# Performance work log

Measured on AMD Instinct MI355X. Metric: run time of the kernel, lower is better.

Reference implementation:

```python
import jax, jax.numpy as jnp
import numpy as np
from jax import lax

B, T, D, H = 128, 129, 128, 64  # batch, window, input_size (num driving series), hidden_size
Tm1 = T - 1


def setup_inputs() -> dict:
    key = jax.random.key(0)
    ks = jax.random.split(key, 11)
    s = 0.05
    return {
        "input_data": jax.random.normal(ks[0], (B, Tm1, D), jnp.float32),
        "W_ehs_w": jax.random.normal(ks[1], (Tm1, 2 * H), jnp.float32) * s,
        "W_ehs_b": jax.random.normal(ks[2], (Tm1,), jnp.float32) * s,
        "U_e_w": jax.random.normal(ks[3], (Tm1, Tm1), jnp.float32) * s,
        "U_e_b": jax.random.normal(ks[4], (Tm1,), jnp.float32) * s,
        "v_e_w": jax.random.normal(ks[5], (1, Tm1), jnp.float32) * s,
        "v_e_b": jax.random.normal(ks[6], (1,), jnp.float32) * s,
        "W_ih": jax.random.normal(ks[7], (4 * H, D), jnp.float32) * s,
        "W_hh": jax.random.normal(ks[8], (4 * H, H), jnp.float32) * s,
        "b_ih": jax.random.normal(ks[9], (4 * H,), jnp.float32) * s,
        "b_hh": jax.random.normal(ks[10], (4 * H,), jnp.float32) * s,
    }


def reference(input_data, W_ehs_w, W_ehs_b, U_e_w, U_e_b, v_e_w, v_e_b, W_ih, W_hh, b_ih, b_hh):
    # input_data: [B, T-1, D]
    dt = input_data.dtype
    # U_e applied to each driving series' full history; constant across t.
    # x_k = input.permute(0,2,1) -> [B, D, T-1]; Linear: x @ W.T + b
    x_perm = jnp.transpose(input_data, (0, 2, 1))            # [B, D, T-1]
    Ue_x = jnp.einsum("bdt,st->bds", x_perm, U_e_w) + U_e_b  # [B, D, T-1]

    def step(carry, x_t):
        h, c = carry                                          # each [B, H]
        # In the torch code (h,c) are broadcast identically over the D axis,
        # so compute W_ehs once per batch row and broadcast.
        hc = jnp.concatenate([h, c], axis=-1)                 # [B, 2H]
        we = hc @ W_ehs_w.T + W_ehs_b                         # [B, T-1]
        z = jnp.tanh(we[:, None, :] + Ue_x)                   # [B, D, T-1]
        v = z @ v_e_w[0] + v_e_b[0]                           # [B, D]
        a = jax.nn.softmax(v, axis=1)                         # softmax over drivers
        x_hat = a * x_t                                       # [B, D]
        # single LSTM step (torch gate order: i, f, g, o)
        gates = x_hat @ W_ih.T + b_ih + h @ W_hh.T + b_hh     # [B, 4H]
        i, f, g, o = jnp.split(gates, 4, axis=1)
        c_new = jax.nn.sigmoid(f) * c + jax.nn.sigmoid(i) * jnp.tanh(g)
        h_new = jax.nn.sigmoid(o) * jnp.tanh(c_new)
        return (h_new, c_new), (x_hat, h_new)

    h0 = jnp.zeros((input_data.shape[0], H), dt)
    c0 = jnp.zeros((input_data.shape[0], H), dt)
    xs = jnp.transpose(input_data, (1, 0, 2))                 # time-major [T-1, B, D]
    _, (xw, he) = lax.scan(step, (h0, c0), xs)
    input_weighted = jnp.transpose(xw, (1, 0, 2))             # [B, T-1, D]
    input_encoded = jnp.transpose(he, (1, 0, 2))              # [B, T-1, H]
    return input_weighted, input_encoded
```

## Files before the change

kernel.cpp:

```cpp
#include <hip/hip_runtime.h>
#include <hip/hip_bf16.h>
#include <hip/hip_fp16.h>

#define NB 128
#define NT 128
#define ND 128
#define NH 64
#define NTH 1024
#define ESTR 144

typedef float f32x2 __attribute__((ext_vector_type(2)));
typedef _Float16 f16x2 __attribute__((ext_vector_type(2)));

__device__ __forceinline__ float fexp2(float x) { return __builtin_amdgcn_exp2f(x); }
__device__ __forceinline__ float frcp (float x) { return __builtin_amdgcn_rcpf(x); }

template<int CTRL>
__device__ __forceinline__ float dppadd(float v) {
  return v + __int_as_float(__builtin_amdgcn_update_dpp(
      0, __float_as_int(v), CTRL, 0xF, 0xF, true));
}
__device__ __forceinline__ float sum16(float v) {
  v = dppadd<0xB1>(v);
  v = dppadd<0x4E>(v);
  v = dppadd<0x141>(v);
  v = dppadd<0x140>(v);
  return v;
}

__device__ __forceinline__ unsigned short f2bf(float f) {
  unsigned u = __float_as_uint(f);
  u += 0x7fffu + ((u >> 16) & 1u);
  return (unsigned short)(u >> 16);
}
__device__ __forceinline__ float blo(unsigned u) { return __uint_as_float(u << 16); }
__device__ __forceinline__ float bhi(unsigned u) { return __uint_as_float(u & 0xffff0000u); }

__device__ __forceinline__ __half2 uh(unsigned u) {
  union { unsigned u; __half2 h; } x; x.u = u; return x.h;
}
__device__ __forceinline__ unsigned hu(__half2 h) {
  union { unsigned u; __half2 h; } x; x.h = h; return x.u;
}
__device__ __forceinline__ f16x2 uh2(unsigned u) {
  union { unsigned u; f16x2 h; } x; x.u = u; return x.h;
}
__device__ __forceinline__ unsigned pkf16(float lo, float hi) {
  return hu(__halves2half2(__float2half_rn(lo), __float2half_rn(hi)));
}

__device__ __forceinline__ float dot2(unsigned a, unsigned b, float c) {
#if __has_builtin(__builtin_amdgcn_fdot2)
  return __builtin_amdgcn_fdot2(uh2(a), uh2(b), c, false);
#else
  const __half2 p = __hmul2(uh(a), uh(b));
  return c + __low2float(p) + __high2float(p);
#endif
}

#define PIN(v) asm volatile("" : "+v"(v))

__global__ __launch_bounds__(NTH)
__attribute__((amdgpu_waves_per_eu(4, 4)))
void darnn_enc(
    const float* __restrict__ x,
    const float* __restrict__ Wehs,
    const float* __restrict__ behs,
    const float* __restrict__ Ue,
    const float* __restrict__ Ueb,
    const float* __restrict__ vew,
    const float* __restrict__ Wih,
    const float* __restrict__ Whh,
    const float* __restrict__ bih,
    const float* __restrict__ bhh,
    float* __restrict__ out)
{
  constexpr float C2  = 2.88539008177792681f;
  constexpr float L2E = 1.44269504088896340f;

  __shared__ __align__(16) float          xh[NT][ND];
  __shared__ __align__(16) unsigned short Ebt[ND][ESTR];
  __shared__ __align__(16) float          hbuf[NT][NH];
  __shared__ __align__(16) unsigned       hcpk[2][8][12];
  __shared__ __align__(16) float          cq[2][16][6];
  __shared__ __align__(16) float          wvm[16][12];
  __shared__ __align__(16) unsigned       xpk[16][12];
  __shared__ __align__(16) float          part64[64];
  __shared__ __align__(16) float          rsb[NT];

  const int b    = blockIdx.x;
  const int tid  = threadIdx.x;
  const int lane = tid & 63;
  const int wid  = tid >> 6;
  const float* xb = x + b * (NT * ND);

#pragma unroll
  for (int i = 0; i < 4; ++i) {
    const int f = i * 1024 + tid;
    const int t = f >> 5, c = (f & 31) << 2;
    *reinterpret_cast<float4*>(&xh[t][c]) =
        *reinterpret_cast<const float4*>(xb + t * ND + c);
  }
  float (*UeTc)[33] = reinterpret_cast<float(*)[33]>(&hbuf[0][0]);
  __syncthreads();

  {
    const int SQ = tid & 31;
    const int DQ = tid >> 5;
    float acc[16];
#pragma unroll
    for (int i = 0; i < 16; ++i) acc[i] = 0.f;
    for (int c = 0; c < 4; ++c) {
      {
        const int ss = 32 * c + DQ;
        const int t4 = 4 * SQ;
        const float4 u4 = *reinterpret_cast<const float4*>(Ue + ss * NT + t4);
        UeTc[t4 + 0][DQ] = u4.x;
        UeTc[t4 + 1][DQ] = u4.y;
        UeTc[t4 + 2][DQ] = u4.z;
        UeTc[t4 + 3][DQ] = u4.w;
      }
      __syncthreads();
#pragma unroll 4
      for (int t = 0; t < NT; ++t) {
        const float4 xv = *reinterpret_cast<const float4*>(&xh[t][4 * DQ]);
        const float u = UeTc[t][SQ];
        acc[4*c+0] = fmaf(xv.x, u, acc[4*c+0]);
        acc[4*c+1] = fmaf(xv.y, u, acc[4*c+1]);
        acc[4*c+2] = fmaf(xv.z, u, acc[4*c+2]);
        acc[4*c+3] = fmaf(xv.w, u, acc[4*c+3]);
      }
      __syncthreads();
    }
#pragma unroll
    for (int c = 0; c < 4; ++c) {
      const int ss = SQ + 32 * c;
      const float ub = Ueb[ss];
#pragma unroll
      for (int di = 0; di < 4; ++di) {
        const float e = fexp2(C2 * (acc[4*c+di] + ub));
        Ebt[4*DQ + di][ss] = f2bf(e);
      }
    }
  }
  __syncthreads();

  if (tid < 192) (&hcpk[0][0][0])[tid] = 0u;
  if (tid < 192) (&cq[0][0][0])[tid] = 0.f;

  const int s_a = tid >> 3, r_a = tid & 7;
  unsigned wehs_p[8];
#pragma unroll
  for (int i = 0; i < 4; ++i) {
    const float4 v4 = *reinterpret_cast<const float4*>(Wehs + s_a * 128 + r_a * 16 + 4 * i);
    wehs_p[2*i]   = pkf16(C2 * v4.x, C2 * v4.y);
    wehs_p[2*i+1] = pkf16(C2 * v4.z, C2 * v4.w);
  }
  float behs_r = C2 * behs[s_a];

  const int s_l = lane & 15;
  const int dp  = lane >> 4;
  const int d0  = 8 * wid + 2 * dp;
  f32x2 mv[4];
  {
    const float4 va = *reinterpret_cast<const float4*>(vew + 8 * s_l);
    const float4 vb = *reinterpret_cast<const float4*>(vew + 8 * s_l + 4);
    const float k = -2.f * L2E;
    mv[0] = (f32x2){k * va.x, k * va.y};
    mv[1] = (f32x2){k * va.z, k * va.w};
    mv[2] = (f32x2){k * vb.x, k * vb.y};
    mv[3] = (f32x2){k * vb.z, k * vb.w};
  }
  f32x2 er2[8];
  {
    const int4 ea = *reinterpret_cast<const int4*>(&Ebt[d0][8 * s_l]);
    const int4 eb = *reinterpret_cast<const int4*>(&Ebt[d0 + 1][8 * s_l]);
    er2[0] = (f32x2){blo((unsigned)ea.x), bhi((unsigned)ea.x)};
    er2[1] = (f32x2){blo((unsigned)ea.y), bhi((unsigned)ea.y)};
    er2[2] = (f32x2){blo((unsigned)ea.z), bhi((unsigned)ea.z)};
    er2[3] = (f32x2){blo((unsigned)ea.w), bhi((unsigned)ea.w)};
    er2[4] = (f32x2){blo((unsigned)eb.x), bhi((unsigned)eb.x)};
    er2[5] = (f32x2){blo((unsigned)eb.y), bhi((unsigned)eb.y)};
    er2[6] = (f32x2){blo((unsigned)eb.z), bhi((unsigned)eb.z)};
    er2[7] = (f32x2){blo((unsigned)eb.w), bhi((unsigned)eb.w)};
  }

  const int kk = lane >> 4, cD = lane & 15;
  const int kD = 4 * wid + kk;
  unsigned wx2[16], wh2[8];
  float b4[4];
#pragma unroll
  for (int g = 0; g < 4; ++g) {
    const int j = 64 * g + kD;
    const float4 u0 = *reinterpret_cast<const float4*>(Wih + j * 128 + 8 * cD);
    const float4 u1 = *reinterpret_cast<const float4*>(Wih + j * 128 + 8 * cD + 4);
    wx2[4*g]   = pkf16(u0.x, u0.y);
    wx2[4*g+1] = pkf16(u0.z, u0.w);
    wx2[4*g+2] = pkf16(u1.x, u1.y);
    wx2[4*g+3] = pkf16(u1.z, u1.w);
    const float4 u2 = *reinterpret_cast<const float4*>(Whh + j * 64 + 4 * cD);
    wh2[2*g]   = pkf16(u2.x, u2.y);
    wh2[2*g+1] = pkf16(u2.z, u2.w);
    b4[g] = bih[j] + bhh[j];
  }

#pragma unroll
  for (int i = 0; i < 8; ++i) PIN(wehs_p[i]);
#pragma unroll
  for (int i = 0; i < 8; ++i) PIN(er2[i]);
#pragma unroll
  for (int i = 0; i < 4; ++i) PIN(mv[i]);
#pragma unroll
  for (int i = 0; i < 16; ++i) PIN(wx2[i]);
#pragma unroll
  for (int i = 0; i < 8; ++i) PIN(wh2[i]);
#pragma unroll
  for (int g = 0; g < 4; ++g) PIN(b4[g]);
  PIN(behs_r);

  __syncthreads();

#define STEP(T, P) do {                                                        \
    const float2 xv = *reinterpret_cast<const float2*>(&xh[(T)][d0]);          \
    float c_old;                                                               \
     {                          \
      const int4 q0 = *reinterpret_cast<const int4*>(&hcpk[(P)][r_a][0]);      \
      const int4 q1 = *reinterpret_cast<const int4*>(&hcpk[(P)][r_a][4]);      \
      c_old = cq[(P)][wid][kk];    \
      float a0 = 0.f, a1 = 0.f;                                                \
      a0 = dot2((unsigned)q0.x, wehs_p[0], a0);                                \
      a1 = dot2((unsigned)q0.y, wehs_p[1], a1);                                \
      a0 = dot2((unsigned)q0.z, wehs_p[2], a0);                                \
      a1 = dot2((unsigned)q0.w, wehs_p[3], a1);                                \
      a0 = dot2((unsigned)q1.x, wehs_p[4], a0);                                \
      a1 = dot2((unsigned)q1.y, wehs_p[5], a1);                                \
      a0 = dot2((unsigned)q1.z, wehs_p[6], a0);                                \
      a1 = dot2((unsigned)q1.w, wehs_p[7], a1);                                \
      float a = a0 + a1;                                                       \
      a = dppadd<0xB1>(a);                                                     \
      a = dppadd<0x4E>(a);                                                     \
      a = dppadd<0x141>(a);                                                    \
      if (r_a == 0) wvm[s_a >> 3][s_a & 7] = fexp2(a + behs_r);                \
    }                                                                          \
    __syncthreads();                                                           \
    int2 hh;                                                                   \
     {                      \
      const float4 wa = *reinterpret_cast<const float4*>(&wvm[s_l][0]);        \
      const float4 wb = *reinterpret_cast<const float4*>(&wvm[s_l][4]);        \
      hh = *reinterpret_cast<const int2*>(&hcpk[(P)][cD >> 2][2 * (cD & 3)]);  \
      const f32x2 one2 = {1.f, 1.f};                                           \
      const f32x2 w01 = {wa.x, wa.y}, w23 = {wa.z, wa.w};                      \
      const f32x2 w45 = {wb.x, wb.y}, w67 = {wb.z, wb.w};                      \
      f32x2 ac0 = {0.f, 0.f}, ac0b = {0.f, 0.f};                               \
      f32x2 ac1 = {0.f, 0.f}, ac1b = {0.f, 0.f};                               \
      BSTEP(w01, er2[0], mv[0], ac0);                                          \
      BSTEP(w23, er2[1], mv[1], ac0b);                                         \
      BSTEP(w45, er2[2], mv[2], ac0);                                          \
      BSTEP(w67, er2[3], mv[3], ac0b);                                         \
      BSTEP(w01, er2[4], mv[0], ac1);                                          \
      BSTEP(w23, er2[5], mv[1], ac1b);                                         \
      BSTEP(w45, er2[6], mv[2], ac1);                                          \
      BSTEP(w67, er2[7], mv[3], ac1b);                                         \
      const f32x2 sv0 = ac0 + ac0b;                                            \
      const f32x2 sv1 = ac1 + ac1b;                                            \
      float s0 = sum16(sv0.x + sv0.y);                                         \
      float s1 = sum16(sv1.x + sv1.y);                                         \
      const float e0 = fexp2(s0);                                              \
      const float e1 = fexp2(s1);                                              \
      if (s_l == 0) {                                                          \
        part64[4 * wid + dp] = e0 + e1;                                        \
        xpk[wid][dp] = pkf16(e0 * xv.x, e1 * xv.y);                            \
        *reinterpret_cast<float2*>(&xh[(T)][d0]) =                             \
            make_float2(e0 * xv.x, e1 * xv.y);                                 \
      }                                                                        \
    }                                                                          \
    __syncthreads();                                                           \
     {     \
      const int4 xq = *reinterpret_cast<const int4*>(&xpk[cD][0]);             \
      float sx[4], sh[4];                                                      \
      _Pragma("unroll")                                                        \
      for (int g = 0; g < 4; ++g) {                                            \
        float s = 0.f;                                                         \
        s = dot2((unsigned)xq.x, wx2[4*g],   s);                               \
        s = dot2((unsigned)xq.y, wx2[4*g+1], s);                               \
        s = dot2((unsigned)xq.z, wx2[4*g+2], s);                               \
        s = dot2((unsigned)xq.w, wx2[4*g+3], s);                               \
        sx[g] = s;                                                             \
        float h = 0.f;                                                         \
        h = dot2((unsigned)hh.x, wh2[2*g],   h);                               \
        h = dot2((unsigned)hh.y, wh2[2*g+1], h);                               \
        sh[g] = h;                                                             \
      }                                                                        \
      float tot = part64[lane];                                                \
      tot = sum16(tot);                                                        \
      tot += __int_as_float(__builtin_amdgcn_ds_swizzle(__float_as_int(tot), 0x401F)); \
      tot += __shfl_xor(tot, 32);                                              \
      const float rs = frcp(tot);                                              \
      float ac[4];                                                             \
      _Pragma("unroll")                                                        \
      for (int g = 0; g < 4; ++g) ac[g] = sum16(fmaf(sx[g], rs, sh[g]));       \
      const float gi = ac[0] + b4[0];                                          \
      const float gf = ac[1] + b4[1];                                          \
      const float gG = ac[2] + b4[2];                                          \
      const float go = ac[3] + b4[3];                                          \
      const float si = frcp(1.f + fexp2(-L2E * gi));                           \
      const float sf = frcp(1.f + fexp2(-L2E * gf));                           \
      const float tg = 1.f - 2.f * frcp(1.f + fexp2(C2 * gG));                 \
      const float cn = fmaf(sf, c_old, si * tg);                               \
      const float so = frcp(1.f + fexp2(-L2E * go));                           \
      const float tc = 1.f - 2.f * frcp(1.f + fexp2(C2 * cn));                 \
      const float hn = so * tc;                                                \
      if (cD == 0) {                                                           \
        __half* Hb = reinterpret_cast<__half*>(&hcpk[(P) ^ 1][0][0]);          \
        Hb[(kD >> 4) * 24 + (kD & 15)]       = __float2half_rn(hn);            \
        Hb[(4 + (kD >> 4)) * 24 + (kD & 15)] = __float2half_rn(cn);            \
        cq[(P) ^ 1][wid][kk] = cn;                                             \
        hbuf[(T)][kD] = hn;                                                    \
      }                                                                        \
      if (tid == 0) rsb[(T)] = rs;                                             \
    }                                                                          \
    __syncthreads();                                                           \
  } while (0)

#define BSTEP(W, E, M, ACC) do {                                   \
    f32x2 q_ = __builtin_elementwise_fma(W, E, one2);              \
    f32x2 r_; r_.x = frcp(q_.x); r_.y = frcp(q_.y);                \
    ACC = __builtin_elementwise_fma(M, r_, ACC);                   \
  } while (0)

  for (int t = 0; t < NT; t += 2) {
    STEP(t, 0);
    STEP(t + 1, 1);
  }
#undef BSTEP
#undef STEP

#pragma unroll
  for (int i = 0; i < 4; ++i) {
    const int f = i * 1024 + tid;
    const int t = f >> 5, c = (f & 31) << 2;
    float4 v = *reinterpret_cast<const float4*>(&xh[t][c]);
    const float rs = rsb[t];
    v.x *= rs; v.y *= rs; v.z *= rs; v.w *= rs;
    *reinterpret_cast<float4*>(out + b * (NT * ND) + t * ND + c) = v;
  }
  float* out2 = out + NB * (NT * ND) + b * (NT * NH);
#pragma unroll
  for (int i = 0; i < 2; ++i) {
    const int f = i * 1024 + tid;
    const int t = f >> 4, c = (f & 15) << 2;
    *reinterpret_cast<float4*>(out2 + t * NH + c) =
        *reinterpret_cast<const float4*>(&hbuf[t][c]);
  }
}

extern "C" void kernel_launch(void* const* d_in, const int* in_sizes, int n_in,
                              void* d_out, int out_size, void* d_ws, size_t ws_size,
                              hipStream_t stream) {
  const float* x    = (const float*)d_in[0];
  const float* Wehs = (const float*)d_in[1];
  const float* behs = (const float*)d_in[2];
  const float* Ue   = (const float*)d_in[3];
  const float* Ueb  = (const float*)d_in[4];
  const float* vew  = (const float*)d_in[5];
  const float* Wih  = (const float*)d_in[7];
  const float* Whh  = (const float*)d_in[8];
  const float* bih  = (const float*)d_in[9];
  const float* bhh  = (const float*)d_in[10];
  float* out = (float*)d_out;

  darnn_enc<<<NB, NTH, 0, stream>>>(x, Wehs, behs, Ue, Ueb, vew, Wih, Whh, bih, bhh, out);
}
```

Baseline: 258.7 us.

## Compute Ue·x directly into per-thread registers, dropping the bf16 LDS staging buffer

The precomputation of exp(2·(U_e x + b)) is restructured. Each thread now computes exactly the (d, s) elements it later needs, using packed f32x2 FMAs. U_e is transposed once into the xh LDS region with a permuted column layout, and x is read straight from global memory. This removes the Ebt bf16 buffer, the bf16 round-trip, and the four chunked passes with their extra barriers. It also keeps the exponentials in full fp32 rather than bf16. The cost is that every thread re-reads x from global/L2 (2 floats per t) and performs redundant work across the lanes that share d.

Result: faster. 250.5 us (-3.2%).

```diff
diff --git a/kernel.cpp b/kernel.cpp
--- a/kernel.cpp
+++ b/kernel.cpp
@@ -7,7 +7,6 @@
 #define ND 128
 #define NH 64
 #define NTH 1024
-#define ESTR 144
 
 typedef float f32x2 __attribute__((ext_vector_type(2)));
 typedef _Float16 f16x2 __attribute__((ext_vector_type(2)));
@@ -27,14 +26,6 @@
   v = dppadd<0x140>(v);
   return v;
 }
-
-__device__ __forceinline__ unsigned short f2bf(float f) {
-  unsigned u = __float_as_uint(f);
-  u += 0x7fffu + ((u >> 16) & 1u);
-  return (unsigned short)(u >> 16);
-}
-__device__ __forceinline__ float blo(unsigned u) { return __uint_as_float(u << 16); }
-__device__ __forceinline__ float bhi(unsigned u) { return __uint_as_float(u & 0xffff0000u); }
 
 __device__ __forceinline__ __half2 uh(unsigned u) {
   union { unsigned u; __half2 h; } x; x.u = u; return x.h;
@@ -79,7 +70,6 @@
   constexpr float L2E = 1.44269504088896340f;
 
   __shared__ __align__(16) float          xh[NT][ND];
-  __shared__ __align__(16) unsigned short Ebt[ND][ESTR];
   __shared__ __align__(16) float          hbuf[NT][NH];
   __shared__ __align__(16) unsigned       hcpk[2][8][12];
   __shared__ __align__(16) float          cq[2][16][6];
@@ -94,6 +84,62 @@
   const int wid  = tid >> 6;
   const float* xb = x + b * (NT * ND);
 
+  const int s_l = lane & 15;
+  const int dp  = lane >> 4;
+  const int d0  = 8 * wid + 2 * dp;
+
+  float (*UeT)[ND] = reinterpret_cast<float(*)[ND]>(&xh[0][0]);
+  {
+    const int s_r = tid & 127;
+    const int t_q = tid >> 7;
+    const int col = 64 * ((s_r >> 2) & 1) + 4 * (s_r >> 3) + (s_r & 3);
+#pragma unroll
+    for (int i = 0; i < 4; ++i) {
+      const int t0 = 4 * (t_q + 8 * i);
+      const float4 u4 = *reinterpret_cast<const float4*>(Ue + s_r * NT + t0);
+      UeT[t0 + 0][col] = u4.x;
+      UeT[t0 + 1][col] = u4.y;
+      UeT[t0 + 2][col] = u4.z;
+      UeT[t0 + 3][col] = u4.w;
+    }
+  }
+  __syncthreads();
+
+  f32x2 er2[8];
+  {
+    const int c0 = 4 * s_l;
+    const int c1 = 64 + 4 * s_l;
+    const float* xg = xb + d0;
+    f32x2 acc2[8];
+#pragma unroll
+    for (int j = 0; j < 8; ++j) acc2[j] = (f32x2){0.f, 0.f};
+    for (int t = 0; t < NT; ++t) {
+      const float2 xv2 = *reinterpret_cast<const float2*>(xg + t * ND);
+      const float4 u0 = *reinterpret_cast<const float4*>(&UeT[t][c0]);
+      const float4 u1 = *reinterpret_cast<const float4*>(&UeT[t][c1]);
+      const f32x2 X = {xv2.x, xv2.y};
+      acc2[0] = __builtin_elementwise_fma(X, (f32x2){u0.x, u0.x}, acc2[0]);
+      acc2[1] = __builtin_elementwise_fma(X, (f32x2){u0.y, u0.y}, acc2[1]);
+      acc2[2] = __builtin_elementwise_fma(X, (f32x2){u0.z, u0.z}, acc2[2]);
+      acc2[3] = __builtin_elementwise_fma(X, (f32x2){u0.w, u0.w}, acc2[3]);
+      acc2[4] = __builtin_elementwise_fma(X, (f32x2){u1.x, u1.x}, acc2[4]);
+      acc2[5] = __builtin_elementwise_fma(X, (f32x2){u1.y, u1.y}, acc2[5]);
+      acc2[6] = __builtin_elementwise_fma(X, (f32x2){u1.z, u1.z}, acc2[6]);
+      acc2[7] = __builtin_elementwise_fma(X, (f32x2){u1.w, u1.w}, acc2[7]);
+    }
+    const float4 ub0 = *reinterpret_cast<const float4*>(Ueb + 8 * s_l);
+    const float4 ub1 = *reinterpret_cast<const float4*>(Ueb + 8 * s_l + 4);
+    er2[0] = (f32x2){fexp2(C2 * (acc2[0].x + ub0.x)), fexp2(C2 * (acc2[1].x + ub0.y))};
+    er2[1] = (f32x2){fexp2(C2 * (acc2[2].x + ub0.z)), fexp2(C2 * (acc2[3].x + ub0.w))};
+    er2[2] = (f32x2){fexp2(C2 * (acc2[4].x + ub1.x)), fexp2(C2 * (acc2[5].x + ub1.y))};
+    er2[3] = (f32x2){fexp2(C2 * (acc2[6].x + ub1.z)), fexp2(C2 * (acc2[7].x + ub1.w))};
+    er2[4] = (f32x2){fexp2(C2 * (acc2[0].y + ub0.x)), fexp2(C2 * (acc2[1].y + ub0.y))};
+    er2[5] = (f32x2){fexp2(C2 * (acc2[2].y + ub0.z)), fexp2(C2 * (acc2[3].y + ub0.w))};
+    er2[6] = (f32x2){fexp2(C2 * (acc2[4].y + ub1.x)), fexp2(C2 * (acc2[5].y + ub1.y))};
+    er2[7] = (f32x2){fexp2(C2 * (acc2[6].y + ub1.z)), fexp2(C2 * (acc2[7].y + ub1.w))};
+  }
+  __syncthreads();
+
 #pragma unroll
   for (int i = 0; i < 4; ++i) {
     const int f = i * 1024 + tid;
@@ -101,49 +147,6 @@
     *reinterpret_cast<float4*>(&xh[t][c]) =
         *reinterpret_cast<const float4*>(xb + t * ND + c);
   }
-  float (*UeTc)[33] = reinterpret_cast<float(*)[33]>(&hbuf[0][0]);
-  __syncthreads();
-
-  {
-    const int SQ = tid & 31;
-    const int DQ = tid >> 5;
-    float acc[16];
-#pragma unroll
-    for (int i = 0; i < 16; ++i) acc[i] = 0.f;
-    for (int c = 0; c < 4; ++c) {
-      {
-        const int ss = 32 * c + DQ;
-        const int t4 = 4 * SQ;
-        const float4 u4 = *reinterpret_cast<const float4*>(Ue + ss * NT + t4);
-        UeTc[t4 + 0][DQ] = u4.x;
-        UeTc[t4 + 1][DQ] = u4.y;
-        UeTc[t4 + 2][DQ] = u4.z;
-        UeTc[t4 + 3][DQ] = u4.w;
-      }
-      __syncthreads();
-#pragma unroll 4
-      for (int t = 0; t < NT; ++t) {
-        const float4 xv = *reinterpret_cast<const float4*>(&xh[t][4 * DQ]);
-        const float u = UeTc[t][SQ];
-        acc[4*c+0] = fmaf(xv.x, u, acc[4*c+0]);
-        acc[4*c+1] = fmaf(xv.y, u, acc[4*c+1]);
-        acc[4*c+2] = fmaf(xv.z, u, acc[4*c+2]);
-        acc[4*c+3] = fmaf(xv.w, u, acc[4*c+3]);
-      }
-      __syncthreads();
-    }
-#pragma unroll
-    for (int c = 0; c < 4; ++c) {
-      const int ss = SQ + 32 * c;
-      const float ub = Ueb[ss];
-#pragma unroll
-      for (int di = 0; di < 4; ++di) {
-        const float e = fexp2(C2 * (acc[4*c+di] + ub));
-        Ebt[4*DQ + di][ss] = f2bf(e);
-      }
-    }
-  }
-  __syncthreads();
 
   if (tid < 192) (&hcpk[0][0][0])[tid] = 0u;
   if (tid < 192) (&cq[0][0][0])[tid] = 0.f;
@@ -158,9 +161,6 @@
   }
   float behs_r = C2 * behs[s_a];
 
-  const int s_l = lane & 15;
-  const int dp  = lane >> 4;
-  const int d0  = 8 * wid + 2 * dp;
   f32x2 mv[4];
   {
     const float4 va = *reinterpret_cast<const float4*>(vew + 8 * s_l);
@@ -170,19 +170,6 @@
     mv[1] = (f32x2){k * va.z, k * va.w};
     mv[2] = (f32x2){k * vb.x, k * vb.y};
     mv[3] = (f32x2){k * vb.z, k * vb.w};
-  }
-  f32x2 er2[8];
-  {
-    const int4 ea = *reinterpret_cast<const int4*>(&Ebt[d0][8 * s_l]);
-    const int4 eb = *reinterpret_cast<const int4*>(&Ebt[d0 + 1][8 * s_l]);
-    er2[0] = (f32x2){blo((unsigned)ea.x), bhi((unsigned)ea.x)};
-    er2[1] = (f32x2){blo((unsigned)ea.y), bhi((unsigned)ea.y)};
-    er2[2] = (f32x2){blo((unsigned)ea.z), bhi((unsigned)ea.z)};
-    er2[3] = (f32x2){blo((unsigned)ea.w), bhi((unsigned)ea.w)};
-    er2[4] = (f32x2){blo((unsigned)eb.x), bhi((unsigned)eb.x)};
-    er2[5] = (f32x2){blo((unsigned)eb.y), bhi((unsigned)eb.y)};
-    er2[6] = (f32x2){blo((unsigned)eb.z), bhi((unsigned)eb.z)};
-    er2[7] = (f32x2){blo((unsigned)eb.w), bhi((unsigned)eb.w)};
   }
 
   const int kk = lane >> 4, cD = lane & 15;
```
